# Optimization experiments

Hardware: AMD Instinct MI355X
Metric: run time of the kernel (lower is better)

The kernel has to match this reference:

```python
import jax, jax.numpy as jnp
import numpy as np

# ---- module hyperparams derived from init_kwargs (see __init__ math) ----
UP, DOWN = 2, 2              # rint(512/256)
UP_TAPS, DOWN_TAPS = 12, 12  # filter_size(6) * factor(2)
PX0, PX1, PY0, PY1 = 9, 8, 9, 8  # pad_total = 17
SLOPE = 0.01


def _firwin_kaiser(numtaps, cutoff, width, fs):
    # scipy.signal.firwin(numtaps, cutoff, width=width, fs=fs) reimplemented:
    # kaiserord attenuation/beta + windowed sinc, normalized to unit DC gain.
    nyq = 0.5 * fs
    atten = 2.285 * (numtaps - 1) * np.pi * (width / nyq) + 7.95
    if atten > 50:
        beta = 0.1102 * (atten - 8.7)
    elif atten > 21:
        beta = 0.5842 * (atten - 21) ** 0.4 + 0.07886 * (atten - 21)
    else:
        beta = 0.0
    m = np.arange(numtaps) - (numtaps - 1) / 2.0
    c = cutoff / nyq
    h = c * np.sinc(c * m) * np.kaiser(numtaps, beta)
    return (h / h.sum()).astype(np.float32)


def setup_inputs() -> dict:
    key = jax.random.key(0)
    x = jax.random.normal(key, (8, 128, 130, 130), dtype=jnp.float32)
    # design_lowpass_filter(numtaps=12, cutoff=100, width=2*28, fs=512) for both
    up_filter = jnp.asarray(_firwin_kaiser(UP_TAPS, 100.0, 56.0, 512.0))
    down_filter = jnp.asarray(_firwin_kaiser(DOWN_TAPS, 100.0, 56.0, 512.0))
    return {"x": x, "up_filter": up_filter, "down_filter": down_filter}


def reference(x, up_filter, down_filter):
    """filtered_lrelu: FIR 2x upsample -> leaky-relu(0.01) -> FIR 2x downsample.

    Matches upfirdn2d(x, fu, up=2, padding=[9,8,9,8], gain=4) ->
    lrelu(slope=0.01, gain=1.0, clamp=None) -> upfirdn2d(x, fd, down=2).
    """
    B, C, H, W = x.shape
    # Separable 1D filters -> 2D outer product. Upsample gain = up**2.
    fu = jnp.outer(up_filter, up_filter) * float(UP * UP)
    fd = jnp.outer(down_filter, down_filter)
    # flip_filter=False in upfirdn2d means true convolution; lax conv is
    # correlation, so flip the (symmetric) kernels explicitly.
    fu = fu[::-1, ::-1][None, None]  # [1,1,kh,kw]
    fd = fd[::-1, ::-1][None, None]
    xr = x.reshape(B * C, 1, H, W)
    # Zero-stuffing upsample via lhs_dilation gives (H-1)*up+1 samples; the
    # reference zero-stuffs to H*up, so add (up-1) zeros to the hi padding.
    y = jax.lax.conv_general_dilated(
        xr, fu, window_strides=(1, 1),
        padding=((PY0, PY1 + UP - 1), (PX0, PX1 + UP - 1)),
        lhs_dilation=(UP, UP))  # [B*C,1,277,277]
    y = jnp.where(y >= 0, y, y * SLOPE)  # leaky relu, gain=1, no clamp
    # Downsample filter + stride-`down` decimation fused in one conv.
    y = jax.lax.conv_general_dilated(
        y, fd, window_strides=(DOWN, DOWN), padding=((0, 0), (0, 0)))
    return y.reshape(B, C, y.shape[-2], y.shape[-1])  # [8,128,128,128]
```

## Files before the change

kernel.cpp:

```cpp
#include <hip/hip_runtime.h>


#define TOX 32
#define TOY 64
#define UST 76
#define U_ROWS 74

template <bool COLSAFE>
__device__ __forceinline__ void stage_a(const float* __restrict__ xc,
                                        float* __restrict__ u_sh,
                                        const float* __restrict__ fu2,
                                        int tid, int ox0, int oy0) {
    const int g   = tid % 19;
    const int h0  = tid / 19;
    const int gc0 = ox0 - 4 + 2 * g;
    bool c0 = true, c2 = true, c4 = true, c6 = true;
    int  o0 = gc0, o2 = gc0 + 2, o4 = gc0 + 4, o6 = gc0 + 6;
    if (!COLSAFE) {
        c0 = (unsigned)(gc0    ) <= 128u; o0 = c0 ? gc0     : 0;
        c2 = (unsigned)(gc0 + 2) <= 128u; o2 = c2 ? gc0 + 2 : 0;
        c4 = (unsigned)(gc0 + 4) <= 128u; o4 = c4 ? gc0 + 4 : 0;
        c6 = (unsigned)(gc0 + 6) <= 129u; o6 = c6 ? gc0 + 6 : 0;
    }
    if (tid < 247) {
#pragma unroll
        for (int k = 0; k < 6; ++k) {
            const int h = h0 + 13 * k;
            if (k < 5 || h < U_ROWS) {
                const int gr = oy0 - 4 + h;
                const bool mayclip = (k == 0 && oy0 == 0) || (k == 5 && oy0 != 0);
                bool rok = true;
                int  grc = gr;
                if (mayclip) { rok = (unsigned)gr < 130u; grc = rok ? gr : 0; }
                const float* __restrict__ xr = xc + grc * 130;
                float2 t01 = *(const float2*)(xr + o0);
                float2 t23 = *(const float2*)(xr + o2);
                float2 t45 = *(const float2*)(xr + o4);
                float  t6  = xr[o6];
                float s0 = t01.x, s1 = t01.y, s2 = t23.x, s3 = t23.y,
                      s4 = t45.x, s5 = t45.y, s6 = t6;
                if (!COLSAFE) {
                    s0 = c0 ? s0 : 0.f; s1 = c0 ? s1 : 0.f;
                    s2 = c2 ? s2 : 0.f; s3 = c2 ? s3 : 0.f;
                    s4 = c4 ? s4 : 0.f; s5 = c4 ? s5 : 0.f;
                    s6 = c6 ? s6 : 0.f;
                }
                float u0 = fu2[0]*s5 + fu2[2]*s4 + fu2[4]*s3 + fu2[6]*s2 + fu2[8]*s1 + fu2[10]*s0;
                float u1 = fu2[1]*s5 + fu2[3]*s4 + fu2[5]*s3 + fu2[7]*s2 + fu2[9]*s1 + fu2[11]*s0;
                float u2 = fu2[0]*s6 + fu2[2]*s5 + fu2[4]*s4 + fu2[6]*s3 + fu2[8]*s2 + fu2[10]*s1;
                float u3 = fu2[1]*s6 + fu2[3]*s5 + fu2[5]*s4 + fu2[7]*s3 + fu2[9]*s2 + fu2[11]*s1;
                if (mayclip && !rok) { u0 = 0.f; u1 = 0.f; u2 = 0.f; u3 = 0.f; }
                *(float4*)(u_sh + h * UST + 4 * g) = make_float4(u0, u1, u2, u3);
            }
        }
    }
}

__global__ __launch_bounds__(256, 7)
void flrelu_fused_kernel(const float* __restrict__ x,
                         const float* __restrict__ upf,
                         const float* __restrict__ downf,
                         float* __restrict__ out) {
    __shared__ __align__(16) float u_s[U_ROWS * UST];

    const int tid = threadIdx.x;
    const int ch  = blockIdx.z;
    const int ox0 = blockIdx.x * TOX;
    const int oy0 = blockIdx.y * TOY;

    float fu2[12], fd[12];
#pragma unroll
    for (int t = 0; t < 12; ++t) fu2[t] = 2.0f * upf[t];
#pragma unroll
    for (int t = 0; t < 12; ++t) fd[t] = downf[11 - t];

    {
        const float* __restrict__ xc = x + (size_t)ch * (130 * 130);
        if (ox0 == 0 || ox0 + TOX == 128)
            stage_a<false>(xc, u_s, fu2, tid, ox0, oy0);
        else
            stage_a<true>(xc, u_s, fu2, tid, ox0, oy0);
    }
    __syncthreads();

    if (tid < 152) {
        const int seg = (tid >= UST) ? 1 : 0;
        const int lj  = tid - seg * UST;
        const float* ucol = u_s + (seg * 32) * UST + lj;
        float*       wb   = u_s + (seg * 42) * UST + lj;
        float rA = ucol[0*UST], rB = ucol[1*UST], rC = ucol[2*UST],
              rD = ucol[3*UST], rE = ucol[4*UST], rF;
        float wA = 0.f, wB = 0.f, wC = 0.f, wD = 0.f, wE = 0.f, wF = 0.f;

#define STEP(m, r0_,r1_,r2_,r3_,r4_,r5_, w0_,w1_,w2_,w3_,w4_,w5_)              \
        {                                                                      \
            r5_ = ucol[(m + 5) * UST];                                         \
            float z0 = fu2[0]*r5_ + fu2[2]*r4_ + fu2[4]*r3_ + fu2[6]*r2_       \
                     + fu2[8]*r1_ + fu2[10]*r0_;                               \
            float z1 = fu2[1]*r5_ + fu2[3]*r4_ + fu2[5]*r3_ + fu2[7]*r2_       \
                     + fu2[9]*r1_ + fu2[11]*r0_;                               \
            z0 = fmaxf(z0, 0.01f * z0);                                        \
            z1 = fmaxf(z1, 0.01f * z1);                                        \
            w0_ = fmaf(fd[0], z0, fd[1] * z1);                                 \
            w1_ = fmaf(fd[2],  z0, fmaf(fd[3],  z1, w1_));                     \
            w2_ = fmaf(fd[4],  z0, fmaf(fd[5],  z1, w2_));                     \
            w3_ = fmaf(fd[6],  z0, fmaf(fd[7],  z1, w3_));                     \
            w4_ = fmaf(fd[8],  z0, fmaf(fd[9],  z1, w4_));                     \
            w5_ = fmaf(fd[10], z0, fmaf(fd[11], z1, w5_));                     \
            if ((m) >= 5) wb[((m) - 5) * UST] = w5_;                           \
        }
#define S6(m0)                                                                 \
        STEP(m0+0, rA,rB,rC,rD,rE,rF, wA,wF,wE,wD,wC,wB)                       \
        STEP(m0+1, rB,rC,rD,rE,rF,rA, wB,wA,wF,wE,wD,wC)                       \
        STEP(m0+2, rC,rD,rE,rF,rA,rB, wC,wB,wA,wF,wE,wD)                       \
        STEP(m0+3, rD,rE,rF,rA,rB,rC, wD,wC,wB,wA,wF,wE)                       \
        STEP(m0+4, rE,rF,rA,rB,rC,rD, wE,wD,wC,wB,wA,wF)                       \
        STEP(m0+5, rF,rA,rB,rC,rD,rE, wF,wE,wD,wC,wB,wA)

        S6(0) S6(6) S6(12) S6(18) S6(24) S6(30)
        STEP(36, rA,rB,rC,rD,rE,rF, wA,wF,wE,wD,wC,wB)
#undef S6
#undef STEP
    }
    __syncthreads();

    {
        const int g = tid & 7;
        const int t = tid >> 3;
        float* __restrict__ outc = out + (size_t)ch * (128 * 128);
#pragma unroll
        for (int oyr = 0; oyr < 2; ++oyr) {
            const float* wr = u_s + (oyr * 42 + t) * UST + 8 * g;
            float4 q0 = *(const float4*)&wr[0];
            float4 q1 = *(const float4*)&wr[4];
            float4 q2 = *(const float4*)&wr[8];
            float4 q3 = *(const float4*)&wr[12];
            float2 e  = *(const float2*)&wr[16];
            float o0v = fd[0]*q0.x + fd[1]*q0.y + fd[2]*q0.z + fd[3]*q0.w
                      + fd[4]*q1.x + fd[5]*q1.y + fd[6]*q1.z + fd[7]*q1.w
                      + fd[8]*q2.x + fd[9]*q2.y + fd[10]*q2.z + fd[11]*q2.w;
            float o1v = fd[0]*q0.z + fd[1]*q0.w + fd[2]*q1.x + fd[3]*q1.y
                      + fd[4]*q1.z + fd[5]*q1.w + fd[6]*q2.x + fd[7]*q2.y
                      + fd[8]*q2.z + fd[9]*q2.w + fd[10]*q3.x + fd[11]*q3.y;
            float o2v = fd[0]*q1.x + fd[1]*q1.y + fd[2]*q1.z + fd[3]*q1.w
                      + fd[4]*q2.x + fd[5]*q2.y + fd[6]*q2.z + fd[7]*q2.w
                      + fd[8]*q3.x + fd[9]*q3.y + fd[10]*q3.z + fd[11]*q3.w;
            float o3v = fd[0]*q1.z + fd[1]*q1.w + fd[2]*q2.x + fd[3]*q2.y
                      + fd[4]*q2.z + fd[5]*q2.w + fd[6]*q3.x + fd[7]*q3.y
                      + fd[8]*q3.z + fd[9]*q3.w + fd[10]*e.x  + fd[11]*e.y;
            *(float4*)(outc + (size_t)(oy0 + oyr * 32 + t) * 128 + ox0 + 4 * g) =
                make_float4(o0v, o1v, o2v, o3v);
        }
    }
}

extern "C" void kernel_launch(void* const* d_in, const int* in_sizes, int n_in,
                              void* d_out, int out_size, void* d_ws, size_t ws_size,
                              hipStream_t stream) {
    const float* x     = (const float*)d_in[0];
    const float* upf   = (const float*)d_in[1];
    const float* downf = (const float*)d_in[2];
    float* out = (float*)d_out;

    dim3 grid(128 / TOX, 128 / TOY, 8 * 128);
    dim3 block(256);
    flrelu_fused_kernel<<<grid, block, 0, stream>>>(x, upf, downf, out);
}
```

Measured before the change: 149.5 us.

## Retile to 26-wide output tiles so stage mappings use power-of-two thread layouts

Shrinks the output tile width from 32 to 26 columns so the upsampled intermediate row fits in 64 floats. That gives clean 16-wide stage-A and 64-wide stage-B thread mappings, fewer shared-memory bytes per block, and a launch bound allowing 8 blocks per CU. The final downsample stage is remapped to 832 tasks of two outputs each, with a bounds check for the ragged last tile. The trade-off is more halo recomputation (five column tiles overlapping instead of four), narrower float2 stores, and partially idle tiles at the right edge.

New measurement: 153.1 us. +2.4%, slower.

```diff
diff --git a/kernel.cpp b/kernel.cpp
--- a/kernel.cpp
+++ b/kernel.cpp
@@ -1,9 +1,9 @@
 #include <hip/hip_runtime.h>
 
 
-#define TOX 32
+#define TOX 26
 #define TOY 64
-#define UST 76
+#define UST 64
 #define U_ROWS 74
 
 template <bool COLSAFE>
@@ -11,8 +11,8 @@
                                         float* __restrict__ u_sh,
                                         const float* __restrict__ fu2,
                                         int tid, int ox0, int oy0) {
-    const int g   = tid % 19;
-    const int h0  = tid / 19;
+    const int g   = tid & 15;
+    const int h0  = tid >> 4;
     const int gc0 = ox0 - 4 + 2 * g;
     bool c0 = true, c2 = true, c4 = true, c6 = true;
     int  o0 = gc0, o2 = gc0 + 2, o4 = gc0 + 4, o6 = gc0 + 6;
@@ -22,41 +22,39 @@
         c4 = (unsigned)(gc0 + 4) <= 128u; o4 = c4 ? gc0 + 4 : 0;
         c6 = (unsigned)(gc0 + 6) <= 129u; o6 = c6 ? gc0 + 6 : 0;
     }
-    if (tid < 247) {
 #pragma unroll
-        for (int k = 0; k < 6; ++k) {
-            const int h = h0 + 13 * k;
-            if (k < 5 || h < U_ROWS) {
-                const int gr = oy0 - 4 + h;
-                const bool mayclip = (k == 0 && oy0 == 0) || (k == 5 && oy0 != 0);
-                bool rok = true;
-                int  grc = gr;
-                if (mayclip) { rok = (unsigned)gr < 130u; grc = rok ? gr : 0; }
-                const float* __restrict__ xr = xc + grc * 130;
-                float2 t01 = *(const float2*)(xr + o0);
-                float2 t23 = *(const float2*)(xr + o2);
-                float2 t45 = *(const float2*)(xr + o4);
-                float  t6  = xr[o6];
-                float s0 = t01.x, s1 = t01.y, s2 = t23.x, s3 = t23.y,
-                      s4 = t45.x, s5 = t45.y, s6 = t6;
-                if (!COLSAFE) {
-                    s0 = c0 ? s0 : 0.f; s1 = c0 ? s1 : 0.f;
-                    s2 = c2 ? s2 : 0.f; s3 = c2 ? s3 : 0.f;
-                    s4 = c4 ? s4 : 0.f; s5 = c4 ? s5 : 0.f;
-                    s6 = c6 ? s6 : 0.f;
-                }
-                float u0 = fu2[0]*s5 + fu2[2]*s4 + fu2[4]*s3 + fu2[6]*s2 + fu2[8]*s1 + fu2[10]*s0;
-                float u1 = fu2[1]*s5 + fu2[3]*s4 + fu2[5]*s3 + fu2[7]*s2 + fu2[9]*s1 + fu2[11]*s0;
-                float u2 = fu2[0]*s6 + fu2[2]*s5 + fu2[4]*s4 + fu2[6]*s3 + fu2[8]*s2 + fu2[10]*s1;
-                float u3 = fu2[1]*s6 + fu2[3]*s5 + fu2[5]*s4 + fu2[7]*s3 + fu2[9]*s2 + fu2[11]*s1;
-                if (mayclip && !rok) { u0 = 0.f; u1 = 0.f; u2 = 0.f; u3 = 0.f; }
-                *(float4*)(u_sh + h * UST + 4 * g) = make_float4(u0, u1, u2, u3);
+    for (int k = 0; k < 5; ++k) {
+        const int h = h0 + 16 * k;
+        if (k < 4 || h < U_ROWS) {
+            const int gr = oy0 - 4 + h;
+            const bool mayclip = (k == 0 && oy0 == 0) || (k == 4 && oy0 != 0);
+            bool rok = true;
+            int  grc = gr;
+            if (mayclip) { rok = (unsigned)gr < 130u; grc = rok ? gr : 0; }
+            const float* __restrict__ xr = xc + grc * 130;
+            float2 t01 = *(const float2*)(xr + o0);
+            float2 t23 = *(const float2*)(xr + o2);
+            float2 t45 = *(const float2*)(xr + o4);
+            float  t6  = xr[o6];
+            float s0 = t01.x, s1 = t01.y, s2 = t23.x, s3 = t23.y,
+                  s4 = t45.x, s5 = t45.y, s6 = t6;
+            if (!COLSAFE) {
+                s0 = c0 ? s0 : 0.f; s1 = c0 ? s1 : 0.f;
+                s2 = c2 ? s2 : 0.f; s3 = c2 ? s3 : 0.f;
+                s4 = c4 ? s4 : 0.f; s5 = c4 ? s5 : 0.f;
+                s6 = c6 ? s6 : 0.f;
             }
+            float u0 = fu2[0]*s5 + fu2[2]*s4 + fu2[4]*s3 + fu2[6]*s2 + fu2[8]*s1 + fu2[10]*s0;
+            float u1 = fu2[1]*s5 + fu2[3]*s4 + fu2[5]*s3 + fu2[7]*s2 + fu2[9]*s1 + fu2[11]*s0;
+            float u2 = fu2[0]*s6 + fu2[2]*s5 + fu2[4]*s4 + fu2[6]*s3 + fu2[8]*s2 + fu2[10]*s1;
+            float u3 = fu2[1]*s6 + fu2[3]*s5 + fu2[5]*s4 + fu2[7]*s3 + fu2[9]*s2 + fu2[11]*s1;
+            if (mayclip && !rok) { u0 = 0.f; u1 = 0.f; u2 = 0.f; u3 = 0.f; }
+            *(float4*)(u_sh + h * UST + 4 * g) = make_float4(u0, u1, u2, u3);
         }
     }
 }
 
-__global__ __launch_bounds__(256, 7)
+__global__ __launch_bounds__(256, 8)
 void flrelu_fused_kernel(const float* __restrict__ x,
                          const float* __restrict__ upf,
                          const float* __restrict__ downf,
@@ -76,16 +74,16 @@
 
     {
         const float* __restrict__ xc = x + (size_t)ch * (130 * 130);
-        if (ox0 == 0 || ox0 + TOX == 128)
+        if (ox0 == 0 || ox0 > 97)
             stage_a<false>(xc, u_s, fu2, tid, ox0, oy0);
         else
             stage_a<true>(xc, u_s, fu2, tid, ox0, oy0);
     }
     __syncthreads();
 
-    if (tid < 152) {
-        const int seg = (tid >= UST) ? 1 : 0;
-        const int lj  = tid - seg * UST;
+    if (tid < 128) {
+        const int seg = tid >> 6;
+        const int lj  = tid & 63;
         const float* ucol = u_s + (seg * 32) * UST + lj;
         float*       wb   = u_s + (seg * 42) * UST + lj;
         float rA = ucol[0*UST], rB = ucol[1*UST], rC = ucol[2*UST],
@@ -125,31 +123,30 @@
     __syncthreads();
 
     {
-        const int g = tid & 7;
-        const int t = tid >> 3;
         float* __restrict__ outc = out + (size_t)ch * (128 * 128);
 #pragma unroll
-        for (int oyr = 0; oyr < 2; ++oyr) {
-            const float* wr = u_s + (oyr * 42 + t) * UST + 8 * g;
-            float4 q0 = *(const float4*)&wr[0];
-            float4 q1 = *(const float4*)&wr[4];
-            float4 q2 = *(const float4*)&wr[8];
-            float4 q3 = *(const float4*)&wr[12];
-            float2 e  = *(const float2*)&wr[16];
-            float o0v = fd[0]*q0.x + fd[1]*q0.y + fd[2]*q0.z + fd[3]*q0.w
-                      + fd[4]*q1.x + fd[5]*q1.y + fd[6]*q1.z + fd[7]*q1.w
-                      + fd[8]*q2.x + fd[9]*q2.y + fd[10]*q2.z + fd[11]*q2.w;
-            float o1v = fd[0]*q0.z + fd[1]*q0.w + fd[2]*q1.x + fd[3]*q1.y
-                      + fd[4]*q1.z + fd[5]*q1.w + fd[6]*q2.x + fd[7]*q2.y
-                      + fd[8]*q2.z + fd[9]*q2.w + fd[10]*q3.x + fd[11]*q3.y;
-            float o2v = fd[0]*q1.x + fd[1]*q1.y + fd[2]*q1.z + fd[3]*q1.w
-                      + fd[4]*q2.x + fd[5]*q2.y + fd[6]*q2.z + fd[7]*q2.w
-                      + fd[8]*q3.x + fd[9]*q3.y + fd[10]*q3.z + fd[11]*q3.w;
-            float o3v = fd[0]*q1.z + fd[1]*q1.w + fd[2]*q2.x + fd[3]*q2.y
-                      + fd[4]*q2.z + fd[5]*q2.w + fd[6]*q3.x + fd[7]*q3.y
-                      + fd[8]*q3.z + fd[9]*q3.w + fd[10]*e.x  + fd[11]*e.y;
-            *(float4*)(outc + (size_t)(oy0 + oyr * 32 + t) * 128 + ox0 + 4 * g) =
-                make_float4(o0v, o1v, o2v, o3v);
+        for (int k = 0; k < 4; ++k) {
+            const int task = tid + 256 * k;
+            if (k < 3 || task < 832) {
+                const int oy   = task / 13;
+                const int j    = task - 13 * oy;
+                const int slot = oy + ((oy >= 32) ? 10 : 0);
+                const float* wr = u_s + slot * UST + 4 * j;
+                float4 q0 = *(const float4*)&wr[0];
+                float4 q1 = *(const float4*)&wr[4];
+                float4 q2 = *(const float4*)&wr[8];
+                float2 e  = *(const float2*)&wr[12];
+                float o0v = fd[0]*q0.x + fd[1]*q0.y + fd[2]*q0.z + fd[3]*q0.w
+                          + fd[4]*q1.x + fd[5]*q1.y + fd[6]*q1.z + fd[7]*q1.w
+                          + fd[8]*q2.x + fd[9]*q2.y + fd[10]*q2.z + fd[11]*q2.w;
+                float o1v = fd[0]*q0.z + fd[1]*q0.w + fd[2]*q1.x + fd[3]*q1.y
+                          + fd[4]*q1.z + fd[5]*q1.w + fd[6]*q2.x + fd[7]*q2.y
+                          + fd[8]*q2.z + fd[9]*q2.w + fd[10]*e.x  + fd[11]*e.y;
+                const int oc = ox0 + 2 * j;
+                if (oc < 128)
+                    *(float2*)(outc + (size_t)(oy0 + oy) * 128 + oc) =
+                        make_float2(o0v, o1v);
+            }
         }
     }
 }
@@ -162,7 +159,7 @@
     const float* downf = (const float*)d_in[2];
     float* out = (float*)d_out;
 
-    dim3 grid(128 / TOX, 128 / TOY, 8 * 128);
+    dim3 grid(5, 128 / TOY, 8 * 128);
     dim3 block(256);
     flrelu_fused_kernel<<<grid, block, 0, stream>>>(x, upf, downf, out);
 }
```

## Exploit filter symmetry and packed float2 FMA in vertical and horizontal passes

Applied to the files above, without the earlier changes.

Exploits the symmetry of the up and down filters to keep only six distinct taps of each, so fewer registers hold filter coefficients. The vertical pass now handles two columns per thread with float2 vector FMAs (intended to map to packed FP32 instructions), halving the active threads there. The horizontal output pass uses paired v2f FMAs and a final horizontal add, and folds the 2x gain factors into one multiply by 4. This assumes the filters are symmetric, which holds for firwin designs, and it leaves fewer threads busy during the vertical pass.

Measured after the change: 149.8 us. No clear change (+0.2%).

```diff
diff --git a/kernel.cpp b/kernel.cpp
--- a/kernel.cpp
+++ b/kernel.cpp
@@ -1,15 +1,23 @@
 #include <hip/hip_runtime.h>
 
+
+typedef float v2f __attribute__((ext_vector_type(2)));
 
 #define TOX 32
 #define TOY 64
 #define UST 76
 #define U_ROWS 74
 
+#define VFMA(a, b, c) __builtin_elementwise_fma((a), (b), (c))
+#define VMAX(a, b)    __builtin_elementwise_max((a), (b))
+
+__device__ __forceinline__ v2f vsp(float s) { return (v2f){s, s}; }
+
 template <bool COLSAFE>
 __device__ __forceinline__ void stage_a(const float* __restrict__ xc,
                                         float* __restrict__ u_sh,
-                                        const float* __restrict__ fu2,
+                                        float e0, float e1, float e2,
+                                        float e3, float e4, float e5,
                                         int tid, int ox0, int oy0) {
     const int g   = tid % 19;
     const int h0  = tid / 19;
@@ -45,10 +53,10 @@
                     s4 = c4 ? s4 : 0.f; s5 = c4 ? s5 : 0.f;
                     s6 = c6 ? s6 : 0.f;
                 }
-                float u0 = fu2[0]*s5 + fu2[2]*s4 + fu2[4]*s3 + fu2[6]*s2 + fu2[8]*s1 + fu2[10]*s0;
-                float u1 = fu2[1]*s5 + fu2[3]*s4 + fu2[5]*s3 + fu2[7]*s2 + fu2[9]*s1 + fu2[11]*s0;
-                float u2 = fu2[0]*s6 + fu2[2]*s5 + fu2[4]*s4 + fu2[6]*s3 + fu2[8]*s2 + fu2[10]*s1;
-                float u3 = fu2[1]*s6 + fu2[3]*s5 + fu2[5]*s4 + fu2[7]*s3 + fu2[9]*s2 + fu2[11]*s1;
+                float u0 = e0*s5 + e1*s4 + e2*s3 + e3*s2 + e4*s1 + e5*s0;
+                float u1 = e5*s5 + e4*s4 + e3*s3 + e2*s2 + e1*s1 + e0*s0;
+                float u2 = e0*s6 + e1*s5 + e2*s4 + e3*s3 + e4*s2 + e5*s1;
+                float u3 = e5*s6 + e4*s5 + e3*s4 + e2*s3 + e1*s2 + e0*s1;
                 if (mayclip && !rok) { u0 = 0.f; u1 = 0.f; u2 = 0.f; u3 = 0.f; }
                 *(float4*)(u_sh + h * UST + 4 * g) = make_float4(u0, u1, u2, u3);
             }
@@ -68,46 +76,47 @@
     const int ox0 = blockIdx.x * TOX;
     const int oy0 = blockIdx.y * TOY;
 
-    float fu2[12], fd[12];
-#pragma unroll
-    for (int t = 0; t < 12; ++t) fu2[t] = 2.0f * upf[t];
-#pragma unroll
-    for (int t = 0; t < 12; ++t) fd[t] = downf[11 - t];
+    const float e0 = upf[0],   e1 = upf[2],   e2 = upf[4],
+                e3 = upf[6],   e4 = upf[8],   e5 = upf[10];
+    const float d0 = downf[0], d1 = downf[1], d2 = downf[2],
+                d3 = downf[3], d4 = downf[4], d5 = downf[5];
 
     {
         const float* __restrict__ xc = x + (size_t)ch * (130 * 130);
         if (ox0 == 0 || ox0 + TOX == 128)
-            stage_a<false>(xc, u_s, fu2, tid, ox0, oy0);
+            stage_a<false>(xc, u_s, e0, e1, e2, e3, e4, e5, tid, ox0, oy0);
         else
-            stage_a<true>(xc, u_s, fu2, tid, ox0, oy0);
+            stage_a<true>(xc, u_s, e0, e1, e2, e3, e4, e5, tid, ox0, oy0);
     }
     __syncthreads();
 
-    if (tid < 152) {
-        const int seg = (tid >= UST) ? 1 : 0;
-        const int lj  = tid - seg * UST;
-        const float* ucol = u_s + (seg * 32) * UST + lj;
-        float*       wb   = u_s + (seg * 42) * UST + lj;
-        float rA = ucol[0*UST], rB = ucol[1*UST], rC = ucol[2*UST],
-              rD = ucol[3*UST], rE = ucol[4*UST], rF;
-        float wA = 0.f, wB = 0.f, wC = 0.f, wD = 0.f, wE = 0.f, wF = 0.f;
+    if (tid < 76) {
+        const int seg = (tid >= 38) ? 1 : 0;
+        const int p   = tid - 38 * seg;
+        const float* ucol = u_s + (seg * 32) * UST + 2 * p;
+        float*       wout = u_s + (seg * 42) * UST + 2 * p;
+        v2f rA = *(const v2f*)(ucol + 0*UST), rB = *(const v2f*)(ucol + 1*UST),
+            rC = *(const v2f*)(ucol + 2*UST), rD = *(const v2f*)(ucol + 3*UST),
+            rE = *(const v2f*)(ucol + 4*UST), rF;
+        v2f wA = vsp(0.f), wB = vsp(0.f), wC = vsp(0.f),
+            wD = vsp(0.f), wE = vsp(0.f), wF = vsp(0.f);
 
 #define STEP(m, r0_,r1_,r2_,r3_,r4_,r5_, w0_,w1_,w2_,w3_,w4_,w5_)              \
         {                                                                      \
-            r5_ = ucol[(m + 5) * UST];                                         \
-            float z0 = fu2[0]*r5_ + fu2[2]*r4_ + fu2[4]*r3_ + fu2[6]*r2_       \
-                     + fu2[8]*r1_ + fu2[10]*r0_;                               \
-            float z1 = fu2[1]*r5_ + fu2[3]*r4_ + fu2[5]*r3_ + fu2[7]*r2_       \
-                     + fu2[9]*r1_ + fu2[11]*r0_;                               \
-            z0 = fmaxf(z0, 0.01f * z0);                                        \
-            z1 = fmaxf(z1, 0.01f * z1);                                        \
-            w0_ = fmaf(fd[0], z0, fd[1] * z1);                                 \
-            w1_ = fmaf(fd[2],  z0, fmaf(fd[3],  z1, w1_));                     \
-            w2_ = fmaf(fd[4],  z0, fmaf(fd[5],  z1, w2_));                     \
-            w3_ = fmaf(fd[6],  z0, fmaf(fd[7],  z1, w3_));                     \
-            w4_ = fmaf(fd[8],  z0, fmaf(fd[9],  z1, w4_));                     \
-            w5_ = fmaf(fd[10], z0, fmaf(fd[11], z1, w5_));                     \
-            if ((m) >= 5) wb[((m) - 5) * UST] = w5_;                           \
+            r5_ = *(const v2f*)(ucol + (m + 5) * UST);                         \
+            v2f z0 = VFMA(vsp(e0), r5_, VFMA(vsp(e1), r4_, VFMA(vsp(e2), r3_, \
+                     VFMA(vsp(e3), r2_, VFMA(vsp(e4), r1_, vsp(e5)*r0_)))));   \
+            v2f z1 = VFMA(vsp(e5), r5_, VFMA(vsp(e4), r4_, VFMA(vsp(e3), r3_, \
+                     VFMA(vsp(e2), r2_, VFMA(vsp(e1), r1_, vsp(e0)*r0_)))));   \
+            z0 = VMAX(z0, 0.01f * z0);                                         \
+            z1 = VMAX(z1, 0.01f * z1);                                         \
+            w0_ = VFMA(vsp(d0), z0, vsp(d1) * z1);                             \
+            w1_ = VFMA(vsp(d2), z0, VFMA(vsp(d3), z1, w1_));                   \
+            w2_ = VFMA(vsp(d4), z0, VFMA(vsp(d5), z1, w2_));                   \
+            w3_ = VFMA(vsp(d5), z0, VFMA(vsp(d4), z1, w3_));                   \
+            w4_ = VFMA(vsp(d3), z0, VFMA(vsp(d2), z1, w4_));                   \
+            w5_ = VFMA(vsp(d1), z0, VFMA(vsp(d0), z1, w5_));                   \
+            if ((m) >= 5) *(v2f*)(wout + ((m) - 5) * UST) = w5_;               \
         }
 #define S6(m0)                                                                 \
         STEP(m0+0, rA,rB,rC,rD,rE,rF, wA,wF,wE,wD,wC,wB)                       \
@@ -127,27 +136,29 @@
     {
         const int g = tid & 7;
         const int t = tid >> 3;
+        const v2f D01 = {d0, d1}, D23 = {d2, d3}, D45 = {d4, d5},
+                  D54 = {d5, d4}, D32 = {d3, d2}, D10 = {d1, d0};
         float* __restrict__ outc = out + (size_t)ch * (128 * 128);
 #pragma unroll
         for (int oyr = 0; oyr < 2; ++oyr) {
             const float* wr = u_s + (oyr * 42 + t) * UST + 8 * g;
-            float4 q0 = *(const float4*)&wr[0];
-            float4 q1 = *(const float4*)&wr[4];
-            float4 q2 = *(const float4*)&wr[8];
-            float4 q3 = *(const float4*)&wr[12];
-            float2 e  = *(const float2*)&wr[16];
-            float o0v = fd[0]*q0.x + fd[1]*q0.y + fd[2]*q0.z + fd[3]*q0.w
-                      + fd[4]*q1.x + fd[5]*q1.y + fd[6]*q1.z + fd[7]*q1.w
-                      + fd[8]*q2.x + fd[9]*q2.y + fd[10]*q2.z + fd[11]*q2.w;
-            float o1v = fd[0]*q0.z + fd[1]*q0.w + fd[2]*q1.x + fd[3]*q1.y
-                      + fd[4]*q1.z + fd[5]*q1.w + fd[6]*q2.x + fd[7]*q2.y
-                      + fd[8]*q2.z + fd[9]*q2.w + fd[10]*q3.x + fd[11]*q3.y;
-            float o2v = fd[0]*q1.x + fd[1]*q1.y + fd[2]*q1.z + fd[3]*q1.w
-                      + fd[4]*q2.x + fd[5]*q2.y + fd[6]*q2.z + fd[7]*q2.w
-                      + fd[8]*q3.x + fd[9]*q3.y + fd[10]*q3.z + fd[11]*q3.w;
-            float o3v = fd[0]*q1.z + fd[1]*q1.w + fd[2]*q2.x + fd[3]*q2.y
-                      + fd[4]*q2.z + fd[5]*q2.w + fd[6]*q3.x + fd[7]*q3.y
-                      + fd[8]*q3.z + fd[9]*q3.w + fd[10]*e.x  + fd[11]*e.y;
+            v2f v0 = *(const v2f*)(wr + 0),  v1 = *(const v2f*)(wr + 2),
+                v2 = *(const v2f*)(wr + 4),  v3 = *(const v2f*)(wr + 6),
+                v4 = *(const v2f*)(wr + 8),  v5 = *(const v2f*)(wr + 10),
+                v6 = *(const v2f*)(wr + 12), v7 = *(const v2f*)(wr + 14),
+                v8 = *(const v2f*)(wr + 16);
+            v2f P0 = VFMA(D01,v0, VFMA(D23,v1, VFMA(D45,v2,
+                     VFMA(D54,v3, VFMA(D32,v4, D10*v5)))));
+            v2f P1 = VFMA(D01,v1, VFMA(D23,v2, VFMA(D45,v3,
+                     VFMA(D54,v4, VFMA(D32,v5, D10*v6)))));
+            v2f P2 = VFMA(D01,v2, VFMA(D23,v3, VFMA(D45,v4,
+                     VFMA(D54,v5, VFMA(D32,v6, D10*v7)))));
+            v2f P3 = VFMA(D01,v3, VFMA(D23,v4, VFMA(D45,v5,
+                     VFMA(D54,v6, VFMA(D32,v7, D10*v8)))));
+            float o0v = 4.0f * (P0.x + P0.y);
+            float o1v = 4.0f * (P1.x + P1.y);
+            float o2v = 4.0f * (P2.x + P2.y);
+            float o3v = 4.0f * (P3.x + P3.y);
             *(float4*)(outc + (size_t)(oy0 + oyr * 32 + t) * 128 + ox0 + 4 * g) =
                 make_float4(o0v, o1v, o2v, o3v);
         }
```
